# Optimization experiments

Measured on AMD Instinct MI355X. Metric: run time of the kernel, lower is better.

The kernel has to match this reference:

```python
import jax, jax.numpy as jnp
import numpy as np

B, N, NFEAT = 64, 384, 16
E = 3
NHID, NOUT = 128, 128
ST_HID, ST_OUT = 64, 16


def _xavier(key, shape, fan_in, fan_out):
    a = jnp.sqrt(6.0 / (fan_in + fan_out))
    return jax.random.uniform(key, shape, jnp.float32, -a, a)


def setup_inputs() -> dict:
    key = jax.random.key(0)
    ks = jax.random.split(key, 10)
    x = jax.random.normal(ks[0], (B, N, NFEAT), jnp.float32)
    adj = jax.random.uniform(ks[1], (B, E, N, N), jnp.float32)
    emb_w = _xavier(ks[2], (NFEAT, NFEAT), NFEAT, NFEAT)            # Linear(nfeat,nfeat,bias=False)
    gc1_w = _xavier(ks[3], (E, NFEAT, NHID), NFEAT, NHID)           # (edge_dim,in,out)
    gc2_w = _xavier(ks[4], (E, NHID, NHID), NHID, NHID)             # single middle layer (num_layers-2=1)
    gc3_w = _xavier(ks[5], (E, NHID, NOUT), NHID, NOUT)
    st_w1 = _xavier(ks[6], (ST_HID, NOUT), NOUT, ST_HID)            # nn.Linear stores (out,in)
    st_b1 = jnp.zeros((ST_HID,), jnp.float32)
    st_w2 = jnp.full((2 * ST_OUT, ST_HID), 1e-10, jnp.float32)      # init.constant_(linear2.weight, 1e-10)
    st_b2 = jnp.zeros((2 * ST_OUT,), jnp.float32)
    rescale_w = jnp.zeros((1,), jnp.float32)                        # Rescale weight init zero
    return {"x": x, "adj": adj, "emb_w": emb_w, "gc1_w": gc1_w, "gc2_w": gc2_w,
            "gc3_w": gc3_w, "st_w1": st_w1, "st_b1": st_b1, "st_w2": st_w2,
            "st_b2": st_b2, "rescale_w": rescale_w}


def _rgcn_layer(h, adj, W, relu):
    # support: einsum('bid,edh->beih'), aggregate: einsum('beij,bejh->beih'), then sum over e
    support = jnp.einsum('bnd,edh->benh', h, W)
    out = jnp.einsum('bemn,benh->bemh', adj, support)
    if relu:
        out = jax.nn.relu(out)
    return out.sum(axis=1)  # aggregate='sum' over edge types


def reference(x, adj, emb_w, gc1_w, gc2_w, gc3_w, st_w1, st_b1, st_w2, st_b2, rescale_w):
    h = x @ emb_w.T                                   # emb Linear, no bias
    h = _rgcn_layer(h, adj, gc1_w, True)
    h = _rgcn_layer(h, adj, gc2_w, True)
    h = _rgcn_layer(h, adj, gc3_w, False)             # gc3: use_relu=False
    flat = h.reshape(-1, h.shape[-1])                 # (B*N, nout)
    z = jnp.tanh(flat @ st_w1.T + st_b1) @ st_w2.T + st_b2
    s, t = z[:, :ST_OUT], z[:, ST_OUT:]
    s = jnp.exp(rescale_w) * jnp.tanh(s)              # Rescale(tanh(s))
    return jnp.stack([s, t])                          # (2, B*N, ST_OUT)
```

## Files before the change

kernel.cpp:

```cpp
#include <hip/hip_runtime.h>
#include <math.h>

#define ROWS 24576
#define ADJ_BE (384*384)

typedef _Float16 h4v __attribute__((ext_vector_type(4)));
typedef _Float16 h8v __attribute__((ext_vector_type(8)));
typedef float f32x4 __attribute__((ext_vector_type(4)));

#define SPLIT_SCALE 2048.0f
#define INV_SPLIT_SCALE (1.0f / 2048.0f)

__global__ __launch_bounds__(256) void k_h0split(const float* __restrict__ x,
        const float* __restrict__ emb_w, _Float16* __restrict__ Hh, _Float16* __restrict__ Hl) {
    __shared__ float embL[256];
    int t = threadIdx.x;
    if (t < 64) *(float4*)&embL[4 * t] = *(const float4*)(emb_w + 4 * t);
    __syncthreads();
    int gid = blockIdx.x * 256 + t;
    int b = gid / 384, r = gid % 384;
    const float* xp = x + (size_t)gid * 16;
    float xr[16];
    *(float4*)&xr[0]  = *(const float4*)(xp);
    *(float4*)&xr[4]  = *(const float4*)(xp + 4);
    *(float4*)&xr[8]  = *(const float4*)(xp + 8);
    *(float4*)&xr[12] = *(const float4*)(xp + 12);
    size_t base = (size_t)b * 16 * 384 + r;
#pragma unroll
    for (int d = 0; d < 16; ++d) {
        float acc = 0.f;
#pragma unroll
        for (int k = 0; k < 16; ++k) acc = fmaf(xr[k], embL[d * 16 + k], acc);
        _Float16 h = (_Float16)acc;
        Hh[base + (size_t)d * 384] = h;
        Hl[base + (size_t)d * 384] = (_Float16)((acc - (float)h) * SPLIT_SCALE);
    }
}

__global__ __launch_bounds__(256) void k_adj16(const float* __restrict__ adj,
        const _Float16* __restrict__ Hh, const _Float16* __restrict__ Hl,
        float* __restrict__ T1) {
    int mt = blockIdx.x, e = blockIdx.y, b = blockIdx.z;
    const float* A = adj + (size_t)(b * 3 + e) * ADJ_BE + (size_t)mt * 64 * 384;
    const _Float16* BH = Hh + (size_t)b * 16 * 384;
    const _Float16* BL = Hl + (size_t)b * 16 * 384;

    __shared__ _Float16 Af[2][4][4][16][8];

    int t = threadIdx.x;
    int wave = t >> 6, lane = t & 63;
    int l16 = lane & 15, quad = lane >> 4;
    int r0s = t >> 3, q4s = t & 7;

    f32x4 acc0 = f32x4{0.f, 0.f, 0.f, 0.f};
    f32x4 acc1 = f32x4{0.f, 0.f, 0.f, 0.f};

    float4 ra[2];
    h8v rbh, rbl;
#pragma unroll
    for (int p = 0; p < 2; ++p)
        ra[p] = *(const float4*)(A + (size_t)(r0s + 32 * p) * 384 + 4 * q4s);
    rbh = *(const h8v*)(BH + (size_t)l16 * 384 + 8 * quad);
    rbl = *(const h8v*)(BL + (size_t)l16 * 384 + 8 * quad);

    for (int kc = 0; kc < 12; ++kc) {
#pragma unroll
        for (int p = 0; p < 2; ++p) {
            int r = r0s + 32 * p;
            float vv[4] = {ra[p].x, ra[p].y, ra[p].z, ra[p].w};
            h4v hh, ll;
#pragma unroll
            for (int c = 0; c < 4; ++c) {
                _Float16 h = (_Float16)vv[c];
                hh[c] = h;
                ll[c] = (_Float16)((vv[c] - (float)h) * SPLIT_SCALE);
            }
            *(h4v*)&Af[0][r >> 4][q4s >> 1][r & 15][(q4s & 1) * 4] = hh;
            *(h4v*)&Af[1][r >> 4][q4s >> 1][r & 15][(q4s & 1) * 4] = ll;
        }
        h8v b_h = rbh, b_l = rbl;
        __syncthreads();
        if (kc + 1 < 12) {
            int kn = (kc + 1) * 32;
#pragma unroll
            for (int p = 0; p < 2; ++p)
                ra[p] = *(const float4*)(A + (size_t)(r0s + 32 * p) * 384 + kn + 4 * q4s);
            rbh = *(const h8v*)(BH + (size_t)l16 * 384 + kn + 8 * quad);
            rbl = *(const h8v*)(BL + (size_t)l16 * 384 + kn + 8 * quad);
        }
        h8v a_h = *(const h8v*)&Af[0][wave][quad][l16][0];
        h8v a_l = *(const h8v*)&Af[1][wave][quad][l16][0];
        acc0 = __builtin_amdgcn_mfma_f32_16x16x32_f16(a_h, b_h, acc0, 0, 0, 0);
        acc1 = __builtin_amdgcn_mfma_f32_16x16x32_f16(a_h, b_l, acc1, 0, 0, 0);
        acc1 = __builtin_amdgcn_mfma_f32_16x16x32_f16(a_l, b_h, acc1, 0, 0, 0);
        __syncthreads();
    }
    float* Tp = T1 + ((size_t)(b * 3 + e) * 384 + (size_t)mt * 64 + wave * 16) * 16;
#pragma unroll
    for (int reg = 0; reg < 4; ++reg) {
        float v = fmaf(acc1[reg], INV_SPLIT_SCALE, acc0[reg]);
        Tp[(quad * 4 + reg) * 16 + l16] = v;
    }
}

__global__ __launch_bounds__(256) void k_l1s2(const float* __restrict__ T1,
        const float* __restrict__ W1, float* __restrict__ h1) {
    __shared__ float wL[3][16][128];
    __shared__ float tL[3][64][17];
    int t = threadIdx.x;
    int rt = blockIdx.x;
    int b = rt / 6, m0 = (rt % 6) * 64;
#pragma unroll
    for (int p = 0; p < 6; ++p) {
        int idx = t + p * 256;
        float4 v = *(const float4*)(W1 + (size_t)idx * 4);
        int e = idx / 512, rem = idx % 512;
        int d = rem >> 5, q = rem & 31;
        *(float4*)&wL[e][d][q * 4] = v;
    }
#pragma unroll
    for (int p = 0; p < 3; ++p) {
        int idx = t + p * 256;
        int e = idx >> 8, rem = idx & 255;
        int r = rem >> 2, q = rem & 3;
        float4 v = *(const float4*)(T1 + ((size_t)(b * 3 + e) * 384 + m0 + r) * 16 + q * 4);
        tL[e][r][q*4+0] = v.x; tL[e][r][q*4+1] = v.y; tL[e][r][q*4+2] = v.z; tL[e][r][q*4+3] = v.w;
    }
    __syncthreads();
    int tx = t & 31;
    int ty = t >> 5;
    float tot[8][4] = {};
#pragma unroll
    for (int e = 0; e < 3; ++e) {
        float acc[8][4] = {};
#pragma unroll
        for (int d = 0; d < 16; ++d) {
            float a[8], w[4];
#pragma unroll
            for (int i = 0; i < 8; ++i) a[i] = tL[e][ty + 8 * i][d];
#pragma unroll
            for (int j = 0; j < 4; ++j) w[j] = wL[e][d][tx + 32 * j];
#pragma unroll
            for (int i = 0; i < 8; ++i)
#pragma unroll
                for (int j = 0; j < 4; ++j)
                    acc[i][j] = fmaf(a[i], w[j], acc[i][j]);
        }
#pragma unroll
        for (int i = 0; i < 8; ++i)
#pragma unroll
            for (int j = 0; j < 4; ++j)
                tot[i][j] += fmaxf(acc[i][j], 0.f);
    }
    float* out = h1 + (size_t)rt * 64 * 128;
#pragma unroll
    for (int i = 0; i < 8; ++i)
#pragma unroll
        for (int j = 0; j < 4; ++j)
            out[(ty + 8 * i) * 128 + tx + 32 * j] = tot[i][j];
}

__global__ __launch_bounds__(256) void k_support(const float* __restrict__ hin,
        const float* __restrict__ W, _Float16* __restrict__ Sh, _Float16* __restrict__ Sl) {
    int rt = blockIdx.x, e = blockIdx.y;
    int b = rt / 6, n0 = (rt % 6) * 64;
    const float* Hp = hin + (size_t)rt * 64 * 128;
    const float* Wp = W + (size_t)e * 128 * 128;
    __shared__ float aT[32][68];
    __shared__ float bT[32][132];
    int t = threadIdx.x;
    int tx = t & 15;
    int ty = t >> 4;
    float acc[4][8] = {};
    for (int k0 = 0; k0 < 128; k0 += 32) {
        __syncthreads();
#pragma unroll
        for (int p = 0; p < 2; ++p) {
            int idx = t + p * 256;
            int r = idx >> 3, q = idx & 7;
            float4 v = *(const float4*)(Hp + (size_t)r * 128 + k0 + q * 4);
            aT[q*4+0][r] = v.x; aT[q*4+1][r] = v.y; aT[q*4+2][r] = v.z; aT[q*4+3][r] = v.w;
        }
#pragma unroll
        for (int p = 0; p < 4; ++p) {
            int idx = t + p * 256;
            int r = idx >> 5, q = idx & 31;
            *(float4*)&bT[r][q * 4] = *(const float4*)(Wp + (size_t)(k0 + r) * 128 + q * 4);
        }
        __syncthreads();
#pragma unroll
        for (int k = 0; k < 32; ++k) {
            float4 av = *(const float4*)&aT[k][4 * ty];
            float4 b0 = *(const float4*)&bT[k][4 * tx];
            float4 b1 = *(const float4*)&bT[k][64 + 4 * tx];
            float a[4] = {av.x, av.y, av.z, av.w};
            float bb[8] = {b0.x, b0.y, b0.z, b0.w, b1.x, b1.y, b1.z, b1.w};
#pragma unroll
            for (int i = 0; i < 4; ++i)
#pragma unroll
                for (int j = 0; j < 8; ++j)
                    acc[i][j] = fmaf(a[i], bb[j], acc[i][j]);
        }
    }
    size_t base = (size_t)(b * 3 + e) * 128 * 384;
#pragma unroll
    for (int j = 0; j < 8; ++j) {
        int n = (j < 4) ? (4 * tx + j) : (64 + 4 * tx + j - 4);
        h4v hh, ll;
#pragma unroll
        for (int i = 0; i < 4; ++i) {
            float v = acc[i][j];
            _Float16 h = (_Float16)v;
            hh[i] = h;
            ll[i] = (_Float16)((v - (float)h) * SPLIT_SCALE);
        }
        size_t off = base + (size_t)n * 384 + n0 + 4 * ty;
        *(h4v*)(Sh + off) = hh;
        *(h4v*)(Sl + off) = ll;
    }
}

template <int RELU>
__global__ __launch_bounds__(256, 3) void k_adj_mfma(const float* __restrict__ adj,
        const _Float16* __restrict__ Sh, const _Float16* __restrict__ Sl,
        float* __restrict__ out) {
    int bid = blockIdx.x;
    int xcd = bid & 7, l = bid >> 3;
    int pair = xcd * 24 + (l >> 2);
    int mt = l & 3;
    int b = pair / 3, e = pair % 3;
    const float* A = adj + (size_t)pair * ADJ_BE + (size_t)mt * 96 * 384;
    const _Float16* Bh = Sh + (size_t)pair * 128 * 384;
    const _Float16* Bl = Sl + (size_t)pair * 128 * 384;
    float* O = out + ((size_t)b * 384 + mt * 96) * 128;

    __shared__ _Float16 Af[2][6][4][16][8];
    __shared__ _Float16 Bf[2][8][4][16][8];

    int t = threadIdx.x;
    int wave = t >> 6, lane = t & 63;
    int l16 = lane & 15, quad = lane >> 4;
    int wm = wave >> 1, wn = wave & 1;
    int r0s = t >> 3, q4s = t & 7;

    f32x4 acc0[3][4], acc1[3][4];
#pragma unroll
    for (int i = 0; i < 3; ++i)
#pragma unroll
        for (int j = 0; j < 4; ++j) {
            acc0[i][j] = f32x4{0.f, 0.f, 0.f, 0.f};
            acc1[i][j] = f32x4{0.f, 0.f, 0.f, 0.f};
        }

    float4 ra[3];
    h8v rb[4];
#pragma unroll
    for (int p = 0; p < 3; ++p)
        ra[p] = *(const float4*)(A + (size_t)(r0s + 32 * p) * 384 + 4 * q4s);
#pragma unroll
    for (int p = 0; p < 4; ++p) {
        int si = t + 256 * (p & 1);
        int n = si >> 2, q8 = si & 3;
        const _Float16* Bsrc = (p < 2) ? Bh : Bl;
        rb[p] = *(const h8v*)(Bsrc + (size_t)n * 384 + 8 * q8);
    }

    for (int k0 = 0; k0 < 384; k0 += 32) {
#pragma unroll
        for (int p = 0; p < 3; ++p) {
            int r = r0s + 32 * p;
            float vv[4] = {ra[p].x, ra[p].y, ra[p].z, ra[p].w};
            h4v hh, ll;
#pragma unroll
            for (int c = 0; c < 4; ++c) {
                _Float16 h = (_Float16)vv[c];
                hh[c] = h;
                ll[c] = (_Float16)((vv[c] - (float)h) * SPLIT_SCALE);
            }
            *(h4v*)&Af[0][r >> 4][q4s >> 1][r & 15][(q4s & 1) * 4] = hh;
            *(h4v*)&Af[1][r >> 4][q4s >> 1][r & 15][(q4s & 1) * 4] = ll;
        }
#pragma unroll
        for (int p = 0; p < 4; ++p) {
            int si = t + 256 * (p & 1);
            int n = si >> 2, q8 = si & 3;
            *(h8v*)&Bf[p >> 1][n >> 4][q8][n & 15][0] = rb[p];
        }
        __syncthreads();
        if (k0 + 32 < 384) {
            int kn = k0 + 32;
#pragma unroll
            for (int p = 0; p < 3; ++p)
                ra[p] = *(const float4*)(A + (size_t)(r0s + 32 * p) * 384 + kn + 4 * q4s);
#pragma unroll
            for (int p = 0; p < 4; ++p) {
                int si = t + 256 * (p & 1);
                int n = si >> 2, q8 = si & 3;
                const _Float16* Bsrc = (p < 2) ? Bh : Bl;
                rb[p] = *(const h8v*)(Bsrc + (size_t)n * 384 + kn + 8 * q8);
            }
        }
        h8v a_h[3], a_l[3];
#pragma unroll
        for (int i = 0; i < 3; ++i) {
            a_h[i] = *(const h8v*)&Af[0][3 * wm + i][quad][l16][0];
            a_l[i] = *(const h8v*)&Af[1][3 * wm + i][quad][l16][0];
        }
#pragma unroll
        for (int j = 0; j < 4; ++j) {
            h8v b_h = *(const h8v*)&Bf[0][4 * wn + j][quad][l16][0];
            h8v b_l = *(const h8v*)&Bf[1][4 * wn + j][quad][l16][0];
#pragma unroll
            for (int i = 0; i < 3; ++i) {
                acc0[i][j] = __builtin_amdgcn_mfma_f32_16x16x32_f16(a_h[i], b_h, acc0[i][j], 0, 0, 0);
                acc1[i][j] = __builtin_amdgcn_mfma_f32_16x16x32_f16(a_h[i], b_l, acc1[i][j], 0, 0, 0);
                acc1[i][j] = __builtin_amdgcn_mfma_f32_16x16x32_f16(a_l[i], b_h, acc1[i][j], 0, 0, 0);
            }
        }
        __syncthreads();
    }
#pragma unroll
    for (int i = 0; i < 3; ++i) {
        int r0 = 48 * wm + 16 * i + quad * 4;
#pragma unroll
        for (int j = 0; j < 4; ++j) {
            int gc = 64 * wn + 16 * j + l16;
#pragma unroll
            for (int reg = 0; reg < 4; ++reg) {
                float v = fmaf(acc1[i][j][reg], INV_SPLIT_SCALE, acc0[i][j][reg]);
                if (RELU) v = fmaxf(v, 0.f);
                atomicAdd(O + (size_t)(r0 + reg) * 128 + gc, v);
            }
        }
    }
}

__global__ void k_zero(float* __restrict__ p, int n4) {
    int i = blockIdx.x * blockDim.x + threadIdx.x;
    if (i < n4) ((float4*)p)[i] = float4{0.f, 0.f, 0.f, 0.f};
}

__global__ __launch_bounds__(256) void k_head(const float* __restrict__ h3,
        const float* __restrict__ st_w1, const float* __restrict__ st_b1,
        const float* __restrict__ st_w2, const float* __restrict__ st_b2,
        const float* __restrict__ rescale_w, float* __restrict__ out) {
    __shared__ float hL[64][132];
    __shared__ float w1L[64][132];
    __shared__ float ytL[64][68];
    __shared__ float w2L[32][68];
    __shared__ float b1L[64], b2L[32];
    int t = threadIdx.x;
    int r0 = blockIdx.x * 64;
#pragma unroll
    for (int p = 0; p < 8; ++p) {
        int idx = t + p * 256;
        int r = idx >> 5, q = idx & 31;
        *(float4*)&hL[r][q * 4] = *(const float4*)(h3 + (size_t)(r0 + r) * 128 + q * 4);
    }
#pragma unroll
    for (int p = 0; p < 8; ++p) {
        int idx = t + p * 256;
        int r = idx >> 5, q = idx & 31;
        *(float4*)&w1L[r][q * 4] = *(const float4*)(st_w1 + (size_t)r * 128 + q * 4);
    }
#pragma unroll
    for (int p = 0; p < 2; ++p) {
        int idx = t + p * 256;
        int r = idx >> 4, q = idx & 15;
        *(float4*)&w2L[r][q * 4] = *(const float4*)(st_w2 + (size_t)r * 64 + q * 4);
    }
    if (t < 64) b1L[t] = st_b1[t];
    else if (t < 96) b2L[t - 64] = st_b2[t - 64];
    __syncthreads();
    int tx = t & 15, ty = t >> 4;
    float acc[4][4] = {};
    for (int d = 0; d < 128; ++d) {
        float a[4], w[4];
#pragma unroll
        for (int i = 0; i < 4; ++i) a[i] = hL[ty + 16 * i][d];
#pragma unroll
        for (int j = 0; j < 4; ++j) w[j] = w1L[tx + 16 * j][d];
#pragma unroll
        for (int i = 0; i < 4; ++i)
#pragma unroll
            for (int j = 0; j < 4; ++j)
                acc[i][j] = fmaf(a[i], w[j], acc[i][j]);
    }
#pragma unroll
    for (int i = 0; i < 4; ++i)
#pragma unroll
        for (int j = 0; j < 4; ++j)
            ytL[ty + 16 * i][tx + 16 * j] = tanhf(acc[i][j] + b1L[tx + 16 * j]);
    __syncthreads();
    int tx8 = t & 7, ty32 = t >> 3;
    float acc2[2][4] = {};
    for (int d = 0; d < 64; ++d) {
        float a[2], w[4];
#pragma unroll
        for (int i = 0; i < 2; ++i) a[i] = ytL[ty32 + 32 * i][d];
#pragma unroll
        for (int j = 0; j < 4; ++j) w[j] = w2L[tx8 + 8 * j][d];
#pragma unroll
        for (int i = 0; i < 2; ++i)
#pragma unroll
            for (int j = 0; j < 4; ++j)
                acc2[i][j] = fmaf(a[i], w[j], acc2[i][j]);
    }
    float er = expf(rescale_w[0]);
#pragma unroll
    for (int i = 0; i < 2; ++i) {
        int r = r0 + ty32 + 32 * i;
#pragma unroll
        for (int j = 0; j < 4; ++j) {
            int c = tx8 + 8 * j;
            float z = acc2[i][j] + b2L[c];
            if (c < 16) out[(size_t)r * 16 + c] = er * tanhf(z);
            else        out[(size_t)(ROWS + r) * 16 + (c - 16)] = z;
        }
    }
}

extern "C" void kernel_launch(void* const* d_in, const int* in_sizes, int n_in,
                              void* d_out, int out_size, void* d_ws, size_t ws_size,
                              hipStream_t stream) {
    const float* x     = (const float*)d_in[0];
    const float* adj   = (const float*)d_in[1];
    const float* emb_w = (const float*)d_in[2];
    const float* gc1   = (const float*)d_in[3];
    const float* gc2   = (const float*)d_in[4];
    const float* gc3   = (const float*)d_in[5];
    const float* st_w1 = (const float*)d_in[6];
    const float* st_b1 = (const float*)d_in[7];
    const float* st_w2 = (const float*)d_in[8];
    const float* st_b2 = (const float*)d_in[9];
    const float* resc  = (const float*)d_in[10];
    float* out = (float*)d_out;
    float* ws  = (float*)d_ws;

    float* T1 = ws;
    float* hA = T1 + 1179648;
    float* hB = hA + 3145728;
    _Float16* Sh = (_Float16*)(hB + 3145728);
    _Float16* Sl = Sh + 9437184;
    _Float16* Hh = (_Float16*)hB;
    _Float16* Hl = Hh + 393216;

    k_h0split<<<96, 256, 0, stream>>>(x, emb_w, Hh, Hl);
    k_adj16<<<dim3(6, 3, 64), 256, 0, stream>>>(adj, Hh, Hl, T1);
    k_l1s2<<<384, 256, 0, stream>>>(T1, gc1, hA);
    k_support<<<dim3(384, 3), 256, 0, stream>>>(hA, gc2, Sh, Sl);
    k_zero<<<3072, 256, 0, stream>>>(hB, 786432);
    k_adj_mfma<1><<<768, 256, 0, stream>>>(adj, Sh, Sl, hB);
    k_support<<<dim3(384, 3), 256, 0, stream>>>(hB, gc3, Sh, Sl);
    k_zero<<<3072, 256, 0, stream>>>(hA, 786432);
    k_adj_mfma<0><<<768, 256, 0, stream>>>(adj, Sh, Sl, hA);
    k_head<<<384, 256, 0, stream>>>(hA, st_w1, st_b1, st_w2, st_b2, resc, out);
}
```

Measured before the change: 438.3 us.

## Load B fragments directly to registers and double-buffer A tile in LDS

```diff
diff --git a/kernel.cpp b/kernel.cpp
--- a/kernel.cpp
+++ b/kernel.cpp
@@ -228,14 +228,13 @@
     int xcd = bid & 7, l = bid >> 3;
     int pair = xcd * 24 + (l >> 2);
     int mt = l & 3;
-    int b = pair / 3, e = pair % 3;
+    int b = pair / 3;
     const float* A = adj + (size_t)pair * ADJ_BE + (size_t)mt * 96 * 384;
     const _Float16* Bh = Sh + (size_t)pair * 128 * 384;
     const _Float16* Bl = Sl + (size_t)pair * 128 * 384;
     float* O = out + ((size_t)b * 384 + mt * 96) * 128;
 
-    __shared__ _Float16 Af[2][6][4][16][8];
-    __shared__ _Float16 Bf[2][8][4][16][8];
+    __shared__ _Float16 Af[2][2][6][4][17][8];
 
     int t = threadIdx.x;
     int wave = t >> 6, lane = t & 63;
@@ -252,72 +251,87 @@
             acc1[i][j] = f32x4{0.f, 0.f, 0.f, 0.f};
         }
 
+    int boff[4];
+#pragma unroll
+    for (int j = 0; j < 4; ++j)
+        boff[j] = (16 * (4 * wn + j) + l16) * 384 + 8 * quad;
+
     float4 ra[3];
-    h8v rb[4];
+    h8v rbh[4], rbl[4];
+
 #pragma unroll
     for (int p = 0; p < 3; ++p)
         ra[p] = *(const float4*)(A + (size_t)(r0s + 32 * p) * 384 + 4 * q4s);
 #pragma unroll
-    for (int p = 0; p < 4; ++p) {
-        int si = t + 256 * (p & 1);
-        int n = si >> 2, q8 = si & 3;
-        const _Float16* Bsrc = (p < 2) ? Bh : Bl;
-        rb[p] = *(const h8v*)(Bsrc + (size_t)n * 384 + 8 * q8);
-    }
-
-    for (int k0 = 0; k0 < 384; k0 += 32) {
-#pragma unroll
-        for (int p = 0; p < 3; ++p) {
-            int r = r0s + 32 * p;
-            float vv[4] = {ra[p].x, ra[p].y, ra[p].z, ra[p].w};
-            h4v hh, ll;
-#pragma unroll
-            for (int c = 0; c < 4; ++c) {
-                _Float16 h = (_Float16)vv[c];
-                hh[c] = h;
-                ll[c] = (_Float16)((vv[c] - (float)h) * SPLIT_SCALE);
-            }
-            *(h4v*)&Af[0][r >> 4][q4s >> 1][r & 15][(q4s & 1) * 4] = hh;
-            *(h4v*)&Af[1][r >> 4][q4s >> 1][r & 15][(q4s & 1) * 4] = ll;
-        }
-#pragma unroll
-        for (int p = 0; p < 4; ++p) {
-            int si = t + 256 * (p & 1);
-            int n = si >> 2, q8 = si & 3;
-            *(h8v*)&Bf[p >> 1][n >> 4][q8][n & 15][0] = rb[p];
+    for (int j = 0; j < 4; ++j) {
+        rbh[j] = *(const h8v*)(Bh + boff[j]);
+        rbl[j] = *(const h8v*)(Bl + boff[j]);
+    }
+#pragma unroll
+    for (int p = 0; p < 3; ++p) {
+        int r = r0s + 32 * p;
+        float vv[4] = {ra[p].x, ra[p].y, ra[p].z, ra[p].w};
+        h4v hh, ll;
+#pragma unroll
+        for (int c = 0; c < 4; ++c) {
+            _Float16 h = (_Float16)vv[c];
+            hh[c] = h;
+            ll[c] = (_Float16)((vv[c] - (float)h) * SPLIT_SCALE);
+        }
+        *(h4v*)&Af[0][0][r >> 4][q4s >> 1][r & 15][(q4s & 1) * 4] = hh;
+        *(h4v*)&Af[0][1][r >> 4][q4s >> 1][r & 15][(q4s & 1) * 4] = ll;
+    }
+#pragma unroll
+    for (int p = 0; p < 3; ++p)
+        ra[p] = *(const float4*)(A + (size_t)(r0s + 32 * p) * 384 + 32 + 4 * q4s);
+    __syncthreads();
+
+    int cur = 0;
+    for (int kc = 0; kc < 12; ++kc) {
+        h8v a_h[3], a_l[3];
+#pragma unroll
+        for (int i = 0; i < 3; ++i) {
+            a_h[i] = *(const h8v*)&Af[cur][0][3 * wm + i][quad][l16][0];
+            a_l[i] = *(const h8v*)&Af[cur][1][3 * wm + i][quad][l16][0];
+        }
+#pragma unroll
+        for (int j = 0; j < 4; ++j)
+#pragma unroll
+            for (int i = 0; i < 3; ++i) {
+                acc0[i][j] = __builtin_amdgcn_mfma_f32_16x16x32_f16(a_h[i], rbh[j], acc0[i][j], 0, 0, 0);
+                acc1[i][j] = __builtin_amdgcn_mfma_f32_16x16x32_f16(a_h[i], rbl[j], acc1[i][j], 0, 0, 0);
+                acc1[i][j] = __builtin_amdgcn_mfma_f32_16x16x32_f16(a_l[i], rbh[j], acc1[i][j], 0, 0, 0);
+            }
+        if (kc + 1 < 12) {
+            int kn = (kc + 1) * 32;
+#pragma unroll
+            for (int j = 0; j < 4; ++j) {
+                rbh[j] = *(const h8v*)(Bh + boff[j] + kn);
+                rbl[j] = *(const h8v*)(Bl + boff[j] + kn);
+            }
+#pragma unroll
+            for (int p = 0; p < 3; ++p) {
+                int r = r0s + 32 * p;
+                float vv[4] = {ra[p].x, ra[p].y, ra[p].z, ra[p].w};
+                h4v hh, ll;
+#pragma unroll
+                for (int c = 0; c < 4; ++c) {
+                    _Float16 h = (_Float16)vv[c];
+                    hh[c] = h;
+                    ll[c] = (_Float16)((vv[c] - (float)h) * SPLIT_SCALE);
+                }
+                *(h4v*)&Af[cur ^ 1][0][r >> 4][q4s >> 1][r & 15][(q4s & 1) * 4] = hh;
+                *(h4v*)&Af[cur ^ 1][1][r >> 4][q4s >> 1][r & 15][(q4s & 1) * 4] = ll;
+            }
+            if (kc + 2 < 12) {
+                int kn2 = (kc + 2) * 32;
+#pragma unroll
+                for (int p = 0; p < 3; ++p)
+                    ra[p] = *(const float4*)(A + (size_t)(r0s + 32 * p) * 384 + kn2 + 4 * q4s);
+            }
         }
         __syncthreads();
-        if (k0 + 32 < 384) {
-            int kn = k0 + 32;
-#pragma unroll
-            for (int p = 0; p < 3; ++p)
-                ra[p] = *(const float4*)(A + (size_t)(r0s + 32 * p) * 384 + kn + 4 * q4s);
-#pragma unroll
-            for (int p = 0; p < 4; ++p) {
-                int si = t + 256 * (p & 1);
-                int n = si >> 2, q8 = si & 3;
-                const _Float16* Bsrc = (p < 2) ? Bh : Bl;
-                rb[p] = *(const h8v*)(Bsrc + (size_t)n * 384 + kn + 8 * q8);
-            }
-        }
-        h8v a_h[3], a_l[3];
-#pragma unroll
-        for (int i = 0; i < 3; ++i) {
-            a_h[i] = *(const h8v*)&Af[0][3 * wm + i][quad][l16][0];
-            a_l[i] = *(const h8v*)&Af[1][3 * wm + i][quad][l16][0];
-        }
-#pragma unroll
-        for (int j = 0; j < 4; ++j) {
-            h8v b_h = *(const h8v*)&Bf[0][4 * wn + j][quad][l16][0];
-            h8v b_l = *(const h8v*)&Bf[1][4 * wn + j][quad][l16][0];
-#pragma unroll
-            for (int i = 0; i < 3; ++i) {
-                acc0[i][j] = __builtin_amdgcn_mfma_f32_16x16x32_f16(a_h[i], b_h, acc0[i][j], 0, 0, 0);
-                acc1[i][j] = __builtin_amdgcn_mfma_f32_16x16x32_f16(a_h[i], b_l, acc1[i][j], 0, 0, 0);
-                acc1[i][j] = __builtin_amdgcn_mfma_f32_16x16x32_f16(a_l[i], b_h, acc1[i][j], 0, 0, 0);
-            }
-        }
-        __syncthreads();
+        cur ^= 1;
     }
 #pragma unroll
     for (int i = 0; i < 3; ++i) {
```

Result: slower. 477.9 us (+9.0%).
